# Kernel tuning notes

Hardware: AMD Instinct MI355X
Metric: run time of the kernel (lower is better)

## Reference

```python
import jax, jax.numpy as jnp
import numpy as np

COST_CLASS, COST_MASK, COST_DICE = 2.0, 5.0, 5.0
NUM_POINTS = 12544

def setup_inputs() -> dict:
    key = jax.random.key(0)
    k1, k2, k3, k4, k5 = jax.random.split(key, 5)
    bs, Q, K = 4, 100, 134
    H = W = 256
    M = 80
    P = H * W
    pred_logits = jax.random.normal(k1, (bs, Q, K), dtype=jnp.float32)
    pred_masks = jax.random.normal(k2, (bs, Q, H, W), dtype=jnp.float32)
    tgt_labels = jax.random.randint(k3, (M,), 0, K - 1, dtype=jnp.int32)
    # binary target masks, stored as float (matches .float() in torch code)
    tgt_masks = (jax.random.uniform(k4, (M, H, W)) > 0.5).astype(jnp.float32)
    # random subset of points without replacement (torch.randperm[:num_points])
    point_idx = jax.random.permutation(k5, P)[:NUM_POINTS].astype(jnp.int32)
    return {"pred_logits": pred_logits, "pred_masks": pred_masks,
            "tgt_labels": tgt_labels, "tgt_masks": tgt_masks,
            "point_idx": point_idx}

def reference(pred_logits, pred_masks, tgt_labels, tgt_masks, point_idx):
    bs, Q, K = pred_logits.shape
    N = bs * Q
    M = tgt_masks.shape[0]
    Pn = point_idx.shape[0]

    # class cost: -p[n, tgt_id[m]]
    out_prob = jax.nn.softmax(pred_logits.reshape(N, K), axis=-1)
    tgt_ids = jnp.clip(tgt_labels.astype(jnp.int32), 0, K - 1)
    cost_class = -out_prob[:, tgt_ids]                      # (N, M)

    # sampled mask logits / targets
    x = pred_masks.reshape(N, -1)[:, point_idx]             # (N, Pn) logits
    y = tgt_masks.reshape(M, -1)[:, point_idx]              # (M, Pn) binary float

    # BCE-with-logits cost, separable form:
    # mean_p[softplus(x) - x*y] = mean_p softplus(x) - (x @ y^T)/Pn
    sp_mean = jnp.mean(jax.nn.softplus(x), axis=-1)         # (N,)
    xy = jnp.einsum('np,mp->nm', x, y)                      # (N, M)
    cost_mask = sp_mean[:, None] - xy / Pn

    # dice cost
    s = jax.nn.sigmoid(x)                                   # (N, Pn)
    numer = 2.0 * jnp.einsum('np,mp->nm', s, y)             # (N, M)
    denom = jnp.sum(s, axis=-1)[:, None] + jnp.sum(y, axis=-1)[None, :]
    cost_dice = 1.0 - (numer + 1.0) / (denom + 1.0)

    C = COST_CLASS * cost_class + COST_MASK * cost_mask + COST_DICE * cost_dice
    return C.reshape(bs, Q, M)
```

## Files before the change

### kernel.cpp

```cpp
#include <hip/hip_runtime.h>
#include <math.h>

#define N_ROWS 400
#define M_ROWS 80
#define K_CLS  134
#define PN     12544
#define PFULL  65536
#define WORDS  (PFULL / 32)
#define NSUB   25
#define KS     64
#define TCH    (WORDS / KS)
#define ITERS  (TCH / 4)
#define NM     (N_ROWS * M_ROWS)
#define YTCH   256

typedef __attribute__((ext_vector_type(4))) float  f32x4;
typedef __attribute__((ext_vector_type(8))) __bf16 bf16x8;

__device__ __forceinline__ float wave_reduce_sum(float v) {
#pragma unroll
    for (int off = 32; off > 0; off >>= 1) v += __shfl_down(v, off, 64);
    return v;
}

__global__ __launch_bounds__(1024) void sort_softmax_kernel(
        const int* __restrict__ point_idx,
        unsigned int* __restrict__ bitmap_g,
        const float* __restrict__ pred_logits,
        float* __restrict__ rowmax, float* __restrict__ rowsum) {
    int tid = threadIdx.x;
    if (blockIdx.x == 0) {
        __shared__ unsigned int bits[WORDS];
        bits[tid] = 0u; bits[tid + 1024] = 0u;
        __syncthreads();
        for (int i = tid; i < PN; i += 1024) {
            int p = point_idx[i];
            atomicOr(&bits[p >> 5], 1u << (p & 31));
        }
        __syncthreads();
        bitmap_g[tid]        = bits[tid];
        bitmap_g[tid + 1024] = bits[tid + 1024];
    } else {
        int wave = tid >> 6, lane = tid & 63;
        int n = (blockIdx.x - 1) * 16 + wave;
        const float* row = pred_logits + n * K_CLS;
        float mx = -1e30f;
        for (int k = lane; k < K_CLS; k += 64) mx = fmaxf(mx, row[k]);
#pragma unroll
        for (int off = 32; off > 0; off >>= 1) mx = fmaxf(mx, __shfl_down(mx, off, 64));
        mx = __shfl(mx, 0, 64);
        float se = 0.f;
        for (int k = lane; k < K_CLS; k += 64) se += expf(row[k] - mx);
        se = wave_reduce_sum(se);
        if (lane == 0) { rowmax[n] = mx; rowsum[n] = se; }
    }
}

__global__ __launch_bounds__(512) void buildY_kernel(
        const float* __restrict__ tgt_masks,
        const unsigned int* __restrict__ bitmap_g,
        bf16x8* __restrict__ Yb, float* __restrict__ ypart) {
    __shared__ float smem[128];
    int b = blockIdx.x;
    int j = b >> 8, tch = b & 255;
    int wave = threadIdx.x >> 6, lane = threadIdx.x & 63;
    int colL = lane & 15, quad = lane >> 4;
    int t = tch * 8 + wave;
    unsigned int w = bitmap_g[t];
    bf16x8 v;
    if (j < 5) {
        int m = 16 * j + colL;
        const float* yrow = tgt_masks + (size_t)m * PFULL + t * 32 + quad * 8;
        f32x4 ya = *(const f32x4*)(yrow);
        f32x4 yc = *(const f32x4*)(yrow + 4);
        float acc = 0.f;
#pragma unroll
        for (int jj = 0; jj < 4; ++jj) {
            float va = ((w >> (quad * 8 + jj)) & 1u)     ? (ya[jj] > 0.5f ? 1.f : 0.f) : 0.f;
            float vc = ((w >> (quad * 8 + jj + 4)) & 1u) ? (yc[jj] > 0.5f ? 1.f : 0.f) : 0.f;
            v[jj] = (__bf16)va; v[jj + 4] = (__bf16)vc;
            acc += va + vc;
        }
        Yb[((size_t)t * 6 + j) * 64 + lane] = v;
        acc += __shfl_down(acc, 32, 64);
        acc += __shfl_down(acc, 16, 64);
        if (quad == 0) smem[wave * 16 + colL] = acc;
        __syncthreads();
        if (threadIdx.x < 16) {
            float s = 0.f;
#pragma unroll
            for (int wv = 0; wv < 8; ++wv) s += smem[wv * 16 + threadIdx.x];
            ypart[tch * M_ROWS + 16 * j + threadIdx.x] = s;
        }
    } else {
#pragma unroll
        for (int jj = 0; jj < 8; ++jj) {
            float sv = (colL == 0 && ((w >> (quad * 8 + jj)) & 1u)) ? 1.f : 0.f;
            v[jj] = (__bf16)sv;
        }
        Yb[((size_t)t * 6 + 5) * 64 + lane] = v;
    }
}

__global__ __launch_bounds__(256, 4) void gemm_full_kernel(
        const float* __restrict__ pred_masks,
        const bf16x8* __restrict__ Yb,
        float* __restrict__ xypart, float* __restrict__ sypart,
        float* __restrict__ rowS, float* __restrict__ rowSP) {
    __shared__ float red[4][20][64];
    __shared__ float rS[4][16], rSP[4][16];
    int tid = threadIdx.x;
    int wave = tid >> 6, lane = tid & 63;
    int colL = lane & 15, quad = lane >> 4;
    int nsub = blockIdx.x % NSUB, ch = blockIdx.x / NSUB;
    int n0 = nsub * 16;
    int t0 = ch * TCH + wave * ITERS;
    const float* rowp = pred_masks + (size_t)(n0 + colL) * PFULL;
    int kbase = t0 * 32 + quad * 8;

    f32x4 accX[5], accS[5];
    f32x4 zero = {0.f, 0.f, 0.f, 0.f};
#pragma unroll
    for (int j = 0; j < 5; ++j) { accX[j] = zero; accS[j] = zero; }
    f32x4 acc5S = zero, acc5P = zero;

    f32x4 PA[3], PB[3];
#pragma unroll
    for (int d = 0; d < 3; ++d) {
        PA[d] = *(const f32x4*)(rowp + kbase + d * 32);
        PB[d] = *(const f32x4*)(rowp + kbase + d * 32 + 4);
    }
    bf16x8 Bc[6], Bn[6];
    {
        const bf16x8* q = Yb + ((size_t)t0 * 6) * 64 + lane;
#pragma unroll
        for (int j = 0; j < 6; ++j) Bc[j] = q[j * 64];
    }

#pragma unroll
    for (int i = 0; i < ITERS; ++i) {
        if (i + 1 < ITERS) {
            const bf16x8* q = Yb + ((size_t)(t0 + i + 1) * 6) * 64 + lane;
#pragma unroll
            for (int j = 0; j < 6; ++j) Bn[j] = q[j * 64];
        }
        f32x4 xa = PA[0], xb = PB[0];
        PA[0] = PA[1]; PB[0] = PB[1];
        PA[1] = PA[2]; PB[1] = PB[2];
        if (i + 3 < ITERS) {
            PA[2] = *(const f32x4*)(rowp + kbase + (i + 3) * 32);
            PB[2] = *(const f32x4*)(rowp + kbase + (i + 3) * 32 + 4);
        }
        float xsv[8];
        *(f32x4*)(xsv) = xa; *(f32x4*)(xsv + 4) = xb;
        bf16x8 aX, aS, aSP;
#pragma unroll
        for (int jj = 0; jj < 8; ++jj) {
            float x  = xsv[jj];
            float ax = fabsf(x);
            float e  = __expf(-ax);
            float den = 1.f + e;
            float inv = __builtin_amdgcn_rcpf(den);
            float sig = (x >= 0.f) ? inv : e * inv;
            float sp  = fmaxf(x, 0.f) + __logf(den);
            aX[jj] = (__bf16)x; aS[jj] = (__bf16)sig; aSP[jj] = (__bf16)sp;
        }
        accX[0] = __builtin_amdgcn_mfma_f32_16x16x32_bf16(aX, Bc[0], accX[0], 0, 0, 0);
        accS[0] = __builtin_amdgcn_mfma_f32_16x16x32_bf16(aS, Bc[0], accS[0], 0, 0, 0);
        accX[1] = __builtin_amdgcn_mfma_f32_16x16x32_bf16(aX, Bc[1], accX[1], 0, 0, 0);
        accS[1] = __builtin_amdgcn_mfma_f32_16x16x32_bf16(aS, Bc[1], accS[1], 0, 0, 0);
        accX[2] = __builtin_amdgcn_mfma_f32_16x16x32_bf16(aX, Bc[2], accX[2], 0, 0, 0);
        accS[2] = __builtin_amdgcn_mfma_f32_16x16x32_bf16(aS, Bc[2], accS[2], 0, 0, 0);
        accX[3] = __builtin_amdgcn_mfma_f32_16x16x32_bf16(aX, Bc[3], accX[3], 0, 0, 0);
        accS[3] = __builtin_amdgcn_mfma_f32_16x16x32_bf16(aS, Bc[3], accS[3], 0, 0, 0);
        accX[4] = __builtin_amdgcn_mfma_f32_16x16x32_bf16(aX, Bc[4], accX[4], 0, 0, 0);
        accS[4] = __builtin_amdgcn_mfma_f32_16x16x32_bf16(aS, Bc[4], accS[4], 0, 0, 0);
        acc5S   = __builtin_amdgcn_mfma_f32_16x16x32_bf16(aS,  Bc[5], acc5S, 0, 0, 0);
        acc5P   = __builtin_amdgcn_mfma_f32_16x16x32_bf16(aSP, Bc[5], acc5P, 0, 0, 0);
#pragma unroll
        for (int j = 0; j < 6; ++j) Bc[j] = Bn[j];
    }

#pragma unroll
    for (int j = 0; j < 5; ++j)
#pragma unroll
        for (int r = 0; r < 4; ++r) red[wave][j * 4 + r][lane] = accX[j][r];
    if (colL == 0) {
#pragma unroll
        for (int r = 0; r < 4; ++r) {
            rS[wave][quad * 4 + r]  = acc5S[r];
            rSP[wave][quad * 4 + r] = acc5P[r];
        }
    }
    __syncthreads();
#pragma unroll
    for (int v0 = 0; v0 < 5; ++v0) {
        int v = wave * 5 + v0;
        float s = red[0][v][lane] + red[1][v][lane] + red[2][v][lane] + red[3][v][lane];
        int j = v >> 2, r = v & 3;
        int n = n0 + quad * 4 + r, m = 16 * j + colL;
        xypart[(size_t)ch * NM + n * M_ROWS + m] = s;
    }
    if (tid < 16) {
        rowS[ch * N_ROWS + n0 + tid] = rS[0][tid] + rS[1][tid] + rS[2][tid] + rS[3][tid];
    } else if (tid < 32) {
        int l = tid - 16;
        rowSP[ch * N_ROWS + n0 + l] = rSP[0][l] + rSP[1][l] + rSP[2][l] + rSP[3][l];
    }
    __syncthreads();
#pragma unroll
    for (int j = 0; j < 5; ++j)
#pragma unroll
        for (int r = 0; r < 4; ++r) red[wave][j * 4 + r][lane] = accS[j][r];
    __syncthreads();
#pragma unroll
    for (int v0 = 0; v0 < 5; ++v0) {
        int v = wave * 5 + v0;
        float s = red[0][v][lane] + red[1][v][lane] + red[2][v][lane] + red[3][v][lane];
        int j = v >> 2, r = v & 3;
        int n = n0 + quad * 4 + r, m = 16 * j + colL;
        sypart[(size_t)ch * NM + n * M_ROWS + m] = s;
    }
}

__global__ void combine_kernel(const float* __restrict__ logits,
                               const int* __restrict__ tgt_labels,
                               const float* __restrict__ rowmax,
                               const float* __restrict__ rowsum,
                               const float* __restrict__ rowS,
                               const float* __restrict__ rowSP,
                               const float* __restrict__ ypart,
                               const float* __restrict__ xypart,
                               const float* __restrict__ sypart,
                               float* __restrict__ out) {
    int idx = blockIdx.x * blockDim.x + threadIdx.x;
    if (idx >= NM) return;
    int n = idx / M_ROWS, m = idx % M_ROWS;
    float xy = 0.f, sy = 0.f, ssumv = 0.f, spsumv = 0.f, ysum = 0.f;
#pragma unroll 8
    for (int g = 0; g < KS; ++g) {
        xy += xypart[(size_t)g * NM + idx];
        sy += sypart[(size_t)g * NM + idx];
        ssumv  += rowS[g * N_ROWS + n];
        spsumv += rowSP[g * N_ROWS + n];
    }
#pragma unroll 16
    for (int g = 0; g < YTCH; ++g) ysum += ypart[g * M_ROWS + m];
    int tid = tgt_labels[m];
    tid = min(max(tid, 0), K_CLS - 1);
    float p = expf(logits[n * K_CLS + tid] - rowmax[n]) / rowsum[n];
    float cost_class = -p;
    float cost_mask = (spsumv - xy) * (1.0f / PN);
    float cost_dice = 1.f - (2.f * sy + 1.f) / (ssumv + ysum + 1.f);
    out[idx] = 2.f * cost_class + 5.f * cost_mask + 5.f * cost_dice;
}

extern "C" void kernel_launch(void* const* d_in, const int* in_sizes, int n_in,
                              void* d_out, int out_size, void* d_ws, size_t ws_size,
                              hipStream_t stream) {
    const float* pred_logits = (const float*)d_in[0];
    const float* pred_masks  = (const float*)d_in[1];
    const int*   tgt_labels  = (const int*)d_in[2];
    const float* tgt_masks   = (const float*)d_in[3];
    const int*   point_idx   = (const int*)d_in[4];
    float* out = (float*)d_out;

    char* ws = (char*)d_ws;
    size_t off = 0;
    auto carve = [&](size_t nbytes) {
        char* p = ws + off;
        off += (nbytes + 255) & ~(size_t)255;
        return p;
    };
    unsigned int* bitmap = (unsigned int*)carve(WORDS * 4);
    bf16x8* Yb    = (bf16x8*)carve((size_t)WORDS * 6 * 64 * 16);
    float* rowmax = (float*)carve(N_ROWS * 4);
    float* rowsum = (float*)carve(N_ROWS * 4);
    float* ypart  = (float*)carve((size_t)YTCH * M_ROWS * 4);
    float* rowS   = (float*)carve((size_t)KS * N_ROWS * 4);
    float* rowSP  = (float*)carve((size_t)KS * N_ROWS * 4);
    float* xypart = (float*)carve((size_t)KS * NM * 4);
    float* sypart = (float*)carve((size_t)KS * NM * 4);
    (void)ws_size; (void)in_sizes; (void)n_in; (void)out_size;

    sort_softmax_kernel<<<26, 1024, 0, stream>>>(point_idx, bitmap,
                                                 pred_logits, rowmax, rowsum);
    buildY_kernel<<<6 * YTCH, 512, 0, stream>>>(tgt_masks, bitmap, Yb, ypart);
    gemm_full_kernel<<<NSUB * KS, 256, 0, stream>>>(
        pred_masks, Yb, xypart, sypart, rowS, rowSP);
    combine_kernel<<<(NM + 255) / 256, 256, 0, stream>>>(
        pred_logits, tgt_labels, rowmax, rowsum, rowS, rowSP, ypart,
        xypart, sypart, out);
}
```

Baseline: 219.5 us.

## Remap GEMM blocks across XCDs, deepen Y prefetch, split combine reduction, atomic ysum

The GEMM block index is remapped so consecutive chunks land on the same XCD (bid&7 interleave), improving L2 locality. The Y operand prefetch is deepened to a two-stage ring buffer loaded after the MFMAs. The combine kernel now splits the 64-way partial reduction across 4 waves with a shared-memory final sum. Per-target y sums are accumulated with atomics instead of 256 partials. These cut latency in the GEMM and the combine tail, at the cost of nondeterministic float atomic ordering.

```diff
diff --git a/kernel.cpp b/kernel.cpp
--- a/kernel.cpp
+++ b/kernel.cpp
@@ -12,7 +12,8 @@
 #define TCH    (WORDS / KS)
 #define ITERS  (TCH / 4)
 #define NM     (N_ROWS * M_ROWS)
-#define YTCH   256
+#define NBLK   (NSUB * KS)
+#define BPX    (NBLK / 8)
 
 typedef __attribute__((ext_vector_type(4))) float  f32x4;
 typedef __attribute__((ext_vector_type(8))) __bf16 bf16x8;
@@ -26,12 +27,14 @@
 __global__ __launch_bounds__(1024) void sort_softmax_kernel(
         const int* __restrict__ point_idx,
         unsigned int* __restrict__ bitmap_g,
+        float* __restrict__ ysum_acc,
         const float* __restrict__ pred_logits,
         float* __restrict__ rowmax, float* __restrict__ rowsum) {
     int tid = threadIdx.x;
     if (blockIdx.x == 0) {
         __shared__ unsigned int bits[WORDS];
         bits[tid] = 0u; bits[tid + 1024] = 0u;
+        if (tid < M_ROWS) ysum_acc[tid] = 0.f;
         __syncthreads();
         for (int i = tid; i < PN; i += 1024) {
             int p = point_idx[i];
@@ -59,7 +62,7 @@
 __global__ __launch_bounds__(512) void buildY_kernel(
         const float* __restrict__ tgt_masks,
         const unsigned int* __restrict__ bitmap_g,
-        bf16x8* __restrict__ Yb, float* __restrict__ ypart) {
+        bf16x8* __restrict__ Yb, float* __restrict__ ysum_acc) {
     __shared__ float smem[128];
     int b = blockIdx.x;
     int j = b >> 8, tch = b & 255;
@@ -90,7 +93,7 @@
             float s = 0.f;
 #pragma unroll
             for (int wv = 0; wv < 8; ++wv) s += smem[wv * 16 + threadIdx.x];
-            ypart[tch * M_ROWS + 16 * j + threadIdx.x] = s;
+            atomicAdd(&ysum_acc[16 * j + threadIdx.x], s);
         }
     } else {
 #pragma unroll
@@ -112,7 +115,9 @@
     int tid = threadIdx.x;
     int wave = tid >> 6, lane = tid & 63;
     int colL = lane & 15, quad = lane >> 4;
-    int nsub = blockIdx.x % NSUB, ch = blockIdx.x / NSUB;
+    int bid = blockIdx.x;
+    int L = (bid & 7) * BPX + (bid >> 3);
+    int nsub = L % NSUB, ch = L / NSUB;
     int n0 = nsub * 16;
     int t0 = ch * TCH + wave * ITERS;
     const float* rowp = pred_masks + (size_t)(n0 + colL) * PFULL;
@@ -130,20 +135,17 @@
         PA[d] = *(const f32x4*)(rowp + kbase + d * 32);
         PB[d] = *(const f32x4*)(rowp + kbase + d * 32 + 4);
     }
-    bf16x8 Bc[6], Bn[6];
-    {
-        const bf16x8* q = Yb + ((size_t)t0 * 6) * 64 + lane;
-#pragma unroll
-        for (int j = 0; j < 6; ++j) Bc[j] = q[j * 64];
+    bf16x8 Bbuf[2][6];
+#pragma unroll
+    for (int s = 0; s < 2; ++s) {
+        const bf16x8* q = Yb + ((size_t)(t0 + s) * 6) * 64 + lane;
+#pragma unroll
+        for (int j = 0; j < 6; ++j) Bbuf[s][j] = q[j * 64];
     }
 
 #pragma unroll
     for (int i = 0; i < ITERS; ++i) {
-        if (i + 1 < ITERS) {
-            const bf16x8* q = Yb + ((size_t)(t0 + i + 1) * 6) * 64 + lane;
-#pragma unroll
-            for (int j = 0; j < 6; ++j) Bn[j] = q[j * 64];
-        }
+        const int s = i & 1;
         f32x4 xa = PA[0], xb = PB[0];
         PA[0] = PA[1]; PB[0] = PB[1];
         PA[1] = PA[2]; PB[1] = PB[2];
@@ -165,20 +167,23 @@
             float sp  = fmaxf(x, 0.f) + __logf(den);
             aX[jj] = (__bf16)x; aS[jj] = (__bf16)sig; aSP[jj] = (__bf16)sp;
         }
-        accX[0] = __builtin_amdgcn_mfma_f32_16x16x32_bf16(aX, Bc[0], accX[0], 0, 0, 0);
-        accS[0] = __builtin_amdgcn_mfma_f32_16x16x32_bf16(aS, Bc[0], accS[0], 0, 0, 0);
-        accX[1] = __builtin_amdgcn_mfma_f32_16x16x32_bf16(aX, Bc[1], accX[1], 0, 0, 0);
-        accS[1] = __builtin_amdgcn_mfma_f32_16x16x32_bf16(aS, Bc[1], accS[1], 0, 0, 0);
-        accX[2] = __builtin_amdgcn_mfma_f32_16x16x32_bf16(aX, Bc[2], accX[2], 0, 0, 0);
-        accS[2] = __builtin_amdgcn_mfma_f32_16x16x32_bf16(aS, Bc[2], accS[2], 0, 0, 0);
-        accX[3] = __builtin_amdgcn_mfma_f32_16x16x32_bf16(aX, Bc[3], accX[3], 0, 0, 0);
-        accS[3] = __builtin_amdgcn_mfma_f32_16x16x32_bf16(aS, Bc[3], accS[3], 0, 0, 0);
-        accX[4] = __builtin_amdgcn_mfma_f32_16x16x32_bf16(aX, Bc[4], accX[4], 0, 0, 0);
-        accS[4] = __builtin_amdgcn_mfma_f32_16x16x32_bf16(aS, Bc[4], accS[4], 0, 0, 0);
-        acc5S   = __builtin_amdgcn_mfma_f32_16x16x32_bf16(aS,  Bc[5], acc5S, 0, 0, 0);
-        acc5P   = __builtin_amdgcn_mfma_f32_16x16x32_bf16(aSP, Bc[5], acc5P, 0, 0, 0);
-#pragma unroll
-        for (int j = 0; j < 6; ++j) Bc[j] = Bn[j];
+        accX[0] = __builtin_amdgcn_mfma_f32_16x16x32_bf16(aX, Bbuf[s][0], accX[0], 0, 0, 0);
+        accS[0] = __builtin_amdgcn_mfma_f32_16x16x32_bf16(aS, Bbuf[s][0], accS[0], 0, 0, 0);
+        accX[1] = __builtin_amdgcn_mfma_f32_16x16x32_bf16(aX, Bbuf[s][1], accX[1], 0, 0, 0);
+        accS[1] = __builtin_amdgcn_mfma_f32_16x16x32_bf16(aS, Bbuf[s][1], accS[1], 0, 0, 0);
+        accX[2] = __builtin_amdgcn_mfma_f32_16x16x32_bf16(aX, Bbuf[s][2], accX[2], 0, 0, 0);
+        accS[2] = __builtin_amdgcn_mfma_f32_16x16x32_bf16(aS, Bbuf[s][2], accS[2], 0, 0, 0);
+        accX[3] = __builtin_amdgcn_mfma_f32_16x16x32_bf16(aX, Bbuf[s][3], accX[3], 0, 0, 0);
+        accS[3] = __builtin_amdgcn_mfma_f32_16x16x32_bf16(aS, Bbuf[s][3], accS[3], 0, 0, 0);
+        accX[4] = __builtin_amdgcn_mfma_f32_16x16x32_bf16(aX, Bbuf[s][4], accX[4], 0, 0, 0);
+        accS[4] = __builtin_amdgcn_mfma_f32_16x16x32_bf16(aS, Bbuf[s][4], accS[4], 0, 0, 0);
+        acc5S   = __builtin_amdgcn_mfma_f32_16x16x32_bf16(aS,  Bbuf[s][5], acc5S, 0, 0, 0);
+        acc5P   = __builtin_amdgcn_mfma_f32_16x16x32_bf16(aSP, Bbuf[s][5], acc5P, 0, 0, 0);
+        if (i + 2 < ITERS) {
+            const bf16x8* q = Yb + ((size_t)(t0 + i + 2) * 6) * 64 + lane;
+#pragma unroll
+            for (int j = 0; j < 6; ++j) Bbuf[s][j] = q[j * 64];
+        }
     }
 
 #pragma unroll
@@ -223,36 +228,46 @@
     }
 }
 
-__global__ void combine_kernel(const float* __restrict__ logits,
-                               const int* __restrict__ tgt_labels,
-                               const float* __restrict__ rowmax,
-                               const float* __restrict__ rowsum,
-                               const float* __restrict__ rowS,
-                               const float* __restrict__ rowSP,
-                               const float* __restrict__ ypart,
-                               const float* __restrict__ xypart,
-                               const float* __restrict__ sypart,
-                               float* __restrict__ out) {
-    int idx = blockIdx.x * blockDim.x + threadIdx.x;
-    if (idx >= NM) return;
+__global__ __launch_bounds__(256) void combine_kernel(
+        const float* __restrict__ logits,
+        const int* __restrict__ tgt_labels,
+        const float* __restrict__ rowmax,
+        const float* __restrict__ rowsum,
+        const float* __restrict__ rowS,
+        const float* __restrict__ rowSP,
+        const float* __restrict__ ysum_acc,
+        const float* __restrict__ xypart,
+        const float* __restrict__ sypart,
+        float* __restrict__ out) {
+    __shared__ float sxy[4][64], ssy[4][64], sss[4][64], ssp[4][64];
+    int il = threadIdx.x & 63, q = threadIdx.x >> 6;
+    int idx = blockIdx.x * 64 + il;
     int n = idx / M_ROWS, m = idx % M_ROWS;
-    float xy = 0.f, sy = 0.f, ssumv = 0.f, spsumv = 0.f, ysum = 0.f;
-#pragma unroll 8
-    for (int g = 0; g < KS; ++g) {
+    float xy = 0.f, sy = 0.f, ss = 0.f, sp = 0.f;
+#pragma unroll
+    for (int gi = 0; gi < 16; ++gi) {
+        int g = q * 16 + gi;
         xy += xypart[(size_t)g * NM + idx];
         sy += sypart[(size_t)g * NM + idx];
-        ssumv  += rowS[g * N_ROWS + n];
-        spsumv += rowSP[g * N_ROWS + n];
-    }
-#pragma unroll 16
-    for (int g = 0; g < YTCH; ++g) ysum += ypart[g * M_ROWS + m];
-    int tid = tgt_labels[m];
-    tid = min(max(tid, 0), K_CLS - 1);
-    float p = expf(logits[n * K_CLS + tid] - rowmax[n]) / rowsum[n];
-    float cost_class = -p;
-    float cost_mask = (spsumv - xy) * (1.0f / PN);
-    float cost_dice = 1.f - (2.f * sy + 1.f) / (ssumv + ysum + 1.f);
-    out[idx] = 2.f * cost_class + 5.f * cost_mask + 5.f * cost_dice;
+        ss += rowS[g * N_ROWS + n];
+        sp += rowSP[g * N_ROWS + n];
+    }
+    sxy[q][il] = xy; ssy[q][il] = sy; sss[q][il] = ss; ssp[q][il] = sp;
+    __syncthreads();
+    if (q == 0) {
+        xy = sxy[0][il] + sxy[1][il] + sxy[2][il] + sxy[3][il];
+        sy = ssy[0][il] + ssy[1][il] + ssy[2][il] + ssy[3][il];
+        ss = sss[0][il] + sss[1][il] + sss[2][il] + sss[3][il];
+        sp = ssp[0][il] + ssp[1][il] + ssp[2][il] + ssp[3][il];
+        float ysum = ysum_acc[m];
+        int tc = tgt_labels[m];
+        tc = min(max(tc, 0), K_CLS - 1);
+        float p = expf(logits[n * K_CLS + tc] - rowmax[n]) / rowsum[n];
+        float cost_class = -p;
+        float cost_mask = (sp - xy) * (1.0f / PN);
+        float cost_dice = 1.f - (2.f * sy + 1.f) / (ss + ysum + 1.f);
+        out[idx] = 2.f * cost_class + 5.f * cost_mask + 5.f * cost_dice;
+    }
 }
 
 extern "C" void kernel_launch(void* const* d_in, const int* in_sizes, int n_in,
@@ -276,19 +291,19 @@
     bf16x8* Yb    = (bf16x8*)carve((size_t)WORDS * 6 * 64 * 16);
     float* rowmax = (float*)carve(N_ROWS * 4);
     float* rowsum = (float*)carve(N_ROWS * 4);
-    float* ypart  = (float*)carve((size_t)YTCH * M_ROWS * 4);
+    float* ysum_acc = (float*)carve(M_ROWS * 4);
     float* rowS   = (float*)carve((size_t)KS * N_ROWS * 4);
     float* rowSP  = (float*)carve((size_t)KS * N_ROWS * 4);
     float* xypart = (float*)carve((size_t)KS * NM * 4);
     float* sypart = (float*)carve((size_t)KS * NM * 4);
     (void)ws_size; (void)in_sizes; (void)n_in; (void)out_size;
 
-    sort_softmax_kernel<<<26, 1024, 0, stream>>>(point_idx, bitmap,
+    sort_softmax_kernel<<<26, 1024, 0, stream>>>(point_idx, bitmap, ysum_acc,
                                                  pred_logits, rowmax, rowsum);
-    buildY_kernel<<<6 * YTCH, 512, 0, stream>>>(tgt_masks, bitmap, Yb, ypart);
-    gemm_full_kernel<<<NSUB * KS, 256, 0, stream>>>(
+    buildY_kernel<<<6 * 256, 512, 0, stream>>>(tgt_masks, bitmap, Yb, ysum_acc);
+    gemm_full_kernel<<<NBLK, 256, 0, stream>>>(
         pred_masks, Yb, xypart, sypart, rowS, rowSP);
-    combine_kernel<<<(NM + 255) / 256, 256, 0, stream>>>(
-        pred_logits, tgt_labels, rowmax, rowsum, rowS, rowSP, ypart,
+    combine_kernel<<<NM / 64, 256, 0, stream>>>(
+        pred_logits, tgt_labels, rowmax, rowsum, rowS, rowSP, ysum_acc,
         xypart, sypart, out);
 }
```

Result: slower. 230.0 us (+4.8%).
